# Optimization experiments

Measured on AMD Instinct MI355X. Metric: run time of the kernel, lower is better.

## Reference

```python
import jax, jax.numpy as jnp
import numpy as np

FEATURE_SIZE = 128
STRIDE = 16
BASE_SIZE = 16
RATIOS = [0.5, 1, 2]
SCALES = [8, 16, 32]


def _generate_anchors(feature_size, stride):
    # Faithful to the torch module's numpy anchor generation (incl. rounding).
    size = BASE_SIZE * BASE_SIZE
    size_ratios = size / np.array(RATIOS)
    ws = np.round(np.sqrt(size_ratios))
    hs = np.round(ws * np.array(RATIOS))
    base = []
    for w, h in zip(ws, hs):
        for s in SCALES:
            base.append([0.0, 0.0, w * s, h * s])
    base = np.array(base)  # [9, 4]
    xo, yo = np.meshgrid(np.arange(feature_size), np.arange(feature_size), indexing='ij')
    # original loop order: x outer, y inner, then 9 base anchors
    centers = np.stack([xo * stride, yo * stride], axis=-1).reshape(-1, 1, 2)  # [F*F,1,2]
    wh = np.broadcast_to(base[None, :, 2:4], (feature_size * feature_size, 9, 2))
    anchors = np.concatenate([np.broadcast_to(centers, wh.shape), wh], axis=-1).reshape(-1, 4)
    return jnp.asarray(anchors, dtype=jnp.float32)  # [F*F*9, 4]


def _conv(x, w, b, pad):
    y = jax.lax.conv_general_dilated(
        x, w, window_strides=(1, 1), padding=[(pad, pad), (pad, pad)],
        dimension_numbers=('NCHW', 'OIHW', 'NCHW'))
    return y + b[None, :, None, None]


def setup_inputs() -> dict:
    key = jax.random.key(0)
    ks = jax.random.split(key, 4)
    F = FEATURE_SIZE
    x = jax.random.normal(ks[0], (1, 1024, F, F), dtype=jnp.float32)
    base_w = jax.random.normal(ks[1], (512, 1024, 3, 3), dtype=jnp.float32) * 0.01
    base_b = jnp.zeros((512,), dtype=jnp.float32)
    cls_w = jax.random.normal(ks[2], (18, 512, 1, 1), dtype=jnp.float32) * 0.01
    cls_b = jnp.zeros((18,), dtype=jnp.float32)
    reg_w = jax.random.normal(ks[3], (36, 512, 1, 1), dtype=jnp.float32) * 0.01
    reg_b = jnp.zeros((36,), dtype=jnp.float32)
    return {"x": x, "base_w": base_w, "base_b": base_b,
            "cls_w": cls_w, "cls_b": cls_b, "reg_w": reg_w, "reg_b": reg_b}


def reference(x, base_w, base_b, cls_w, cls_b, reg_w, reg_b):
    F = FEATURE_SIZE
    anchors = _generate_anchors(F, STRIDE)  # [N,4], N = F*F*9

    rpn_conv = jax.nn.relu(_conv(x, base_w, base_b, pad=1))        # [1,512,F,F]
    rpn_cls = _conv(rpn_conv, cls_w, cls_b, pad=0)                  # [1,18,F,F]
    # softmax over the 2-way fg/bg axis after reshape, as in the original
    cls_rs = rpn_cls.reshape(1, 2, 9 * F, F)
    cls_prob = jax.nn.softmax(cls_rs, axis=1).reshape(1, 18, F, F)
    rpn_reg = _conv(rpn_conv, reg_w, reg_b, pad=0)                  # [1,36,F,F]

    cls = jnp.transpose(cls_prob, (0, 2, 3, 1)).reshape(-1, 2)      # [N,2]
    reg = jnp.transpose(rpn_reg, (0, 2, 3, 1)).reshape(-1, 4)       # [N,4]

    # Vectorized decode — faithful to the original per-anchor loop math:
    # p0 = ax + aw*d0 ; p1 = ay + ah*d1 ; p2 = aw + exp(d2) ; p3 = ah + exp(d3)
    p0 = anchors[:, 0] + anchors[:, 2] * reg[:, 0]
    p1 = anchors[:, 1] + anchors[:, 3] * reg[:, 1]
    p2 = anchors[:, 2] + jnp.exp(reg[:, 2])
    p3 = anchors[:, 3] + jnp.exp(reg[:, 3])
    proposals = jnp.stack([p0, p1, p2, p3], axis=-1)                # [N,4]
    scores = cls[:, 1]                                              # [N]
    return jnp.concatenate([proposals, scores[:, None]], axis=-1)   # [N,5]
```

## Files before the change

### kernel.cpp

```cpp
#include <hip/hip_runtime.h>
#include <hip/hip_bf16.h>

typedef unsigned short u16;
typedef short s4v __attribute__((ext_vector_type(4)));
typedef short s8v __attribute__((ext_vector_type(8)));
typedef float f4v __attribute__((ext_vector_type(4)));

#define F 128
#define CIN 1024
#define CMID 512
#define XP 130
#define K9 9216

#define A_ELEMS 8704
#define B_ELEMS 8192
#define AOFF(b) ((b) * A_ELEMS)
#define BOFF(b) (2 * A_ELEMS + (b) * B_ELEMS)

__device__ __forceinline__ u16 f2bf(float v) {
    union { float f; unsigned u; } x; x.f = v;
    unsigned r = x.u + 0x7fff + ((x.u >> 16) & 1);
    return (u16)(r >> 16);
}

__device__ __forceinline__ void gl16(const u16* g, u16* l) {
    __builtin_amdgcn_global_load_lds(
        (const __attribute__((address_space(1))) void*)g,
        (__attribute__((address_space(3))) void*)l,
        16, 0, 0);
}

__constant__ float WBASE[9] = {184.f, 368.f, 736.f, 128.f, 256.f, 512.f,  88.f, 176.f, 352.f};
__constant__ float HBASE[9] = { 96.f, 192.f, 384.f, 128.f, 256.f, 512.f, 176.f, 352.f, 704.f};

__global__ __launch_bounds__(256) void prep_all(
    const float* __restrict__ x, const float* __restrict__ bw,
    const float* __restrict__ cls_w, const float* __restrict__ reg_w,
    u16* __restrict__ xpad, u16* __restrict__ wt, u16* __restrict__ wc) {
    __shared__ u16 ldsT[64 * 132];
    const int b = blockIdx.x;
    const int tid = threadIdx.x;

    if (b < 2048) {
        const int h  = b >> 4;
        const int cb = (b & 15) * 64;
        {
            const int L = tid & 31, cl = tid >> 5;
            const int w4 = L * 4;
            #pragma unroll
            for (int p = 0; p < 8; ++p) {
                const int c = p * 8 + cl;
                f4v v = *(const f4v*)&x[(cb + c) * (F * F) + h * F + w4];
                s4v pk;
                #pragma unroll
                for (int k = 0; k < 4; ++k) pk[k] = (short)f2bf(v[k]);
                *(s4v*)&ldsT[c * 132 + w4] = pk;
            }
        }
        __syncthreads();
        {
            const int cs = (tid & 7) * 8;
            const int wb = tid >> 3;
            #pragma unroll
            for (int p = 0; p < 4; ++p) {
                const int w = p * 32 + wb;
                s8v o;
                #pragma unroll
                for (int j = 0; j < 8; ++j) o[j] = (short)ldsT[(cs + j) * 132 + w];
                *(s8v*)&xpad[((h + 1) * XP + (w + 1)) * CIN + cb + cs] = o;
            }
        }
    } else if (b < 2560) {
        const int oc = b - 2048;
        #pragma unroll 1
        for (int p = 0; p < 4; ++p) {
            const int c = p * 256 + tid;
            const float* src = bw + oc * K9 + c * 9;
            #pragma unroll
            for (int q = 0; q < 9; ++q)
                wt[oc * K9 + q * 1024 + c] = f2bf(src[q]);
        }
    } else if (b < 2818) {
        int t = (b - 2560) * 256 + tid;
        int cell = t >> 7, c8 = (t & 127) * 8;
        int h, w;
        if (cell < 130)      { h = 0;   w = cell; }
        else if (cell < 260) { h = 129; w = cell - 130; }
        else { int rm = cell - 260; h = 1 + (rm >> 1); w = (rm & 1) * 129; }
        s8v z = {};
        *(s8v*)&xpad[(h * XP + w) * CIN + c8] = z;
    } else {
        int t = (b - 2818) * 256 + tid;
        int oc = t >> 9, c = t & 511;
        float v = 0.f;
        if (oc < 18)      v = cls_w[oc * 512 + c];
        else if (oc < 54) v = reg_w[(oc - 18) * 512 + c];
        wc[t] = f2bf(v);
    }
}

__global__ __launch_bounds__(256, 2) void gemm_conv(
    const u16* __restrict__ xpad, const u16* __restrict__ wt,
    const float* __restrict__ bias, u16* __restrict__ rpn) {
    __shared__ u16 smem[2 * A_ELEMS + 2 * B_ELEMS];
    const int tid = threadIdx.x;
    const int w_id = (blockIdx.x & 7) * 64 + (blockIdx.x >> 3);
    const int oc0 = ((w_id & 7) >> 1) * 128;
    const int gh  = (w_id >> 3) * 2 + (w_id & 1);

    const int lane = tid & 63;
    const int wv = tid >> 6;
    const int lm = lane & 15;
    const int lq = lane >> 4;
    const int wm = (wv >> 1) * 64;
    const int wn = (wv & 1) * 64;

    const int sw = (lane & 7) ^ ((lane >> 3) & 7);
    const u16* pA = xpad + (lane >> 3) * CIN + sw * 8;
    const u16* pB = wt + (size_t)(oc0 + wv * 32 + (lane >> 3)) * K9 + sw * 8;

    f4v acc[4][4] = {};

    auto issueA = [&](int ms) {
        const int dy = ms >> 4, cc = ms & 15;
        const u16* src = pA + ((gh + dy) * XP) * CIN + cc * 64;
        u16* dst = &smem[AOFF(ms & 1)];
        #pragma unroll
        for (int jj = 0; jj < 4; ++jj) {
            const int ci = wv * 4 + jj;
            gl16(src + ci * 8 * CIN, dst + ci * 512);
        }
        if (wv == 0) gl16(src + 16 * 8 * CIN, dst + 16 * 512);
    };
    auto issueB = [&](int ms, int dx, int buf) {
        const int dy = ms >> 4, cc = ms & 15;
        const int dydx = dy * 3 + dx;
        const u16* src = pB + dydx * CIN + cc * 64;
        u16* dst = &smem[BOFF(buf) + wv * 32 * 64];
        #pragma unroll
        for (int jj = 0; jj < 4; ++jj)
            gl16(src + jj * 8 * K9, dst + jj * 8 * 64);
    };

    issueA(0);
    issueB(0, 0, 0);

    for (int ms = 0; ms < 48; ++ms) {
        const u16* Ab = &smem[AOFF(ms & 1)];
        #pragma unroll
        for (int dx = 0; dx < 3; ++dx) {
            const int t = ms * 3 + dx;

            if (dx == 1) {
                if (ms < 47) {
                    if (wv == 0) asm volatile("s_waitcnt vmcnt(5)" ::: "memory");
                    else         asm volatile("s_waitcnt vmcnt(4)" ::: "memory");
                } else {
                    asm volatile("s_waitcnt vmcnt(0)" ::: "memory");
                }
            } else {
                asm volatile("s_waitcnt vmcnt(0)" ::: "memory");
            }
            __builtin_amdgcn_s_barrier();

            if (t + 1 < 144) {
                const int msn = (dx == 2) ? ms + 1 : ms;
                const int dxn = (dx == 2) ? 0 : dx + 1;
                issueB(msn, dxn, (t + 1) & 1);
            }
            if (dx == 0 && ms + 1 < 48) issueA(ms + 1);

            const u16* Bb = &smem[BOFF(t & 1)];
            #pragma unroll
            for (int kk = 0; kk < 2; ++kk) {
                const int kseg = kk * 4 + lq;
                s8v af[4], bfr[4];
                #pragma unroll
                for (int i = 0; i < 4; ++i) {
                    const int ra = wm + i * 16 + lm + dx;
                    const int rb = wn + i * 16 + lm;
                    af[i]  = *(const s8v*)&Ab[ra * 64 + ((kseg ^ (ra & 7)) << 3)];
                    bfr[i] = *(const s8v*)&Bb[rb * 64 + ((kseg ^ (rb & 7)) << 3)];
                }
                #pragma unroll
                for (int mi = 0; mi < 4; ++mi)
                    #pragma unroll
                    for (int ni = 0; ni < 4; ++ni)
                        acc[mi][ni] = __builtin_amdgcn_mfma_f32_16x16x32_bf16(
                            af[mi], bfr[ni], acc[mi][ni], 0, 0, 0);
            }
        }
    }

    #pragma unroll
    for (int ni = 0; ni < 4; ++ni) {
        const int oc = oc0 + wn + ni * 16 + lm;
        const float bv = bias[oc];
        #pragma unroll
        for (int mi = 0; mi < 4; ++mi) {
            #pragma unroll
            for (int rr = 0; rr < 4; ++rr) {
                const int m = wm + mi * 16 + lq * 4 + rr;
                float v = acc[mi][ni][rr] + bv;
                v = v > 0.f ? v : 0.f;
                rpn[(gh * 128 + m) * CMID + oc] = f2bf(v);
            }
        }
    }
}

__global__ __launch_bounds__(256) void stage23(
    const u16* __restrict__ rpn, const u16* __restrict__ wc,
    const float* __restrict__ cls_b, const float* __restrict__ reg_b,
    float* __restrict__ out) {
    __shared__ float part[4][32][65];
    const int tid = threadIdx.x, lane = tid & 63, wv = tid >> 6;
    const int lm = lane & 15, lq = lane >> 4;
    const int m0 = blockIdx.x * 32;

    #pragma unroll
    for (int g = 0; g < 2; ++g) {
        f4v acc[4] = {};
        const u16* arow = rpn + (m0 + g * 16 + lm) * CMID + wv * 128 + lq * 8;
        const u16* brow = wc + lm * CMID + wv * 128 + lq * 8;
        #pragma unroll
        for (int k = 0; k < 4; ++k) {
            s8v af = *(const s8v*)(arow + k * 32);
            #pragma unroll
            for (int ni = 0; ni < 4; ++ni) {
                s8v bf = *(const s8v*)(brow + ni * 16 * CMID + k * 32);
                acc[ni] = __builtin_amdgcn_mfma_f32_16x16x32_bf16(af, bf, acc[ni], 0, 0, 0);
            }
        }
        #pragma unroll
        for (int ni = 0; ni < 4; ++ni)
            #pragma unroll
            for (int rr = 0; rr < 4; ++rr)
                part[wv][g * 16 + lq * 4 + rr][ni * 16 + lm] = acc[ni][rr];
    }
    __syncthreads();

    float vsum[8];
    const int col = tid & 63, rb = tid >> 6;
    const float bv = col < 18 ? cls_b[col] : (col < 54 ? reg_b[col - 18] : 0.f);
    #pragma unroll
    for (int rr = 0; rr < 8; ++rr) {
        const int row = rb * 8 + rr;
        vsum[rr] = part[0][row][col] + part[1][row][col]
                 + part[2][row][col] + part[3][row][col] + bv;
    }
    __syncthreads();
    #pragma unroll
    for (int rr = 0; rr < 8; ++rr)
        part[0][rb * 8 + rr][col] = vsum[rr];
    __syncthreads();

    #pragma unroll 1
    for (int g = 0; g < 2; ++g) {
        if (tid < 144) {
            const int pl0 = tid / 9, a = tid - pl0 * 9;
            const int pl = g * 16 + pl0;
            const float* v = part[0][pl];
            const int ch = 2 * a + 1;
            const int pair = (ch < 9) ? ch + 9 : ch - 9;
            const float score = 1.f / (1.f + expf(v[pair] - v[ch]));
            const float r0 = v[18 + 4 * a], r1 = v[19 + 4 * a];
            const float r2 = v[20 + 4 * a], r3 = v[21 + 4 * a];
            const float wb = WBASE[a], hb = HBASE[a];
            const int p = m0 + pl;
            const int h = p >> 7, w = p & 127;
            float* o = out + (p * 9 + a) * 5;
            o[0] = h * 16.f + wb * r0;
            o[1] = w * 16.f + hb * r1;
            o[2] = wb + expf(r2);
            o[3] = hb + expf(r3);
            o[4] = score;
        }
    }
}

extern "C" void kernel_launch(void* const* d_in, const int* in_sizes, int n_in,
                              void* d_out, int out_size, void* d_ws, size_t ws_size,
                              hipStream_t stream) {
    const float* x      = (const float*)d_in[0];
    const float* base_w = (const float*)d_in[1];
    const float* base_b = (const float*)d_in[2];
    const float* cls_w  = (const float*)d_in[3];
    const float* cls_b  = (const float*)d_in[4];
    const float* reg_w  = (const float*)d_in[5];
    const float* reg_b  = (const float*)d_in[6];
    float* out = (float*)d_out;

    char* ws = (char*)d_ws;
    u16* xpad = (u16*)ws;
    u16* wt   = (u16*)(ws + 34611200);
    u16* wc   = (u16*)(ws + 34611200 + 9437184);
    u16* rpn  = (u16*)(ws + 34611200 + 9437184 + 65536);

    prep_all<<<2946, 256, 0, stream>>>(x, base_w, cls_w, reg_w, xpad, wt, wc);
    gemm_conv<<<512, 256, 0, stream>>>(xpad, wt, base_b, rpn);
    stage23<<<512, 256, 0, stream>>>(rpn, wc, cls_b, reg_b, out);
}
```

Before: 257.2 us.

## Fuse 1x1 head stage into conv GEMM via last-block-per-row atomic counter

```diff
diff --git a/kernel.cpp b/kernel.cpp
--- a/kernel.cpp
+++ b/kernel.cpp
@@ -36,7 +36,8 @@
 __global__ __launch_bounds__(256) void prep_all(
     const float* __restrict__ x, const float* __restrict__ bw,
     const float* __restrict__ cls_w, const float* __restrict__ reg_w,
-    u16* __restrict__ xpad, u16* __restrict__ wt, u16* __restrict__ wc) {
+    u16* __restrict__ xpad, u16* __restrict__ wt, u16* __restrict__ wc,
+    unsigned* __restrict__ cnt, int doTail) {
     __shared__ u16 ldsT[64 * 132];
     const int b = blockIdx.x;
     const int tid = threadIdx.x;
@@ -96,127 +97,16 @@
         if (oc < 18)      v = cls_w[oc * 512 + c];
         else if (oc < 54) v = reg_w[(oc - 18) * 512 + c];
         wc[t] = f2bf(v);
-    }
-}
-
-__global__ __launch_bounds__(256, 2) void gemm_conv(
-    const u16* __restrict__ xpad, const u16* __restrict__ wt,
-    const float* __restrict__ bias, u16* __restrict__ rpn) {
-    __shared__ u16 smem[2 * A_ELEMS + 2 * B_ELEMS];
-    const int tid = threadIdx.x;
-    const int w_id = (blockIdx.x & 7) * 64 + (blockIdx.x >> 3);
-    const int oc0 = ((w_id & 7) >> 1) * 128;
-    const int gh  = (w_id >> 3) * 2 + (w_id & 1);
-
-    const int lane = tid & 63;
-    const int wv = tid >> 6;
-    const int lm = lane & 15;
-    const int lq = lane >> 4;
-    const int wm = (wv >> 1) * 64;
-    const int wn = (wv & 1) * 64;
-
-    const int sw = (lane & 7) ^ ((lane >> 3) & 7);
-    const u16* pA = xpad + (lane >> 3) * CIN + sw * 8;
-    const u16* pB = wt + (size_t)(oc0 + wv * 32 + (lane >> 3)) * K9 + sw * 8;
-
-    f4v acc[4][4] = {};
-
-    auto issueA = [&](int ms) {
-        const int dy = ms >> 4, cc = ms & 15;
-        const u16* src = pA + ((gh + dy) * XP) * CIN + cc * 64;
-        u16* dst = &smem[AOFF(ms & 1)];
-        #pragma unroll
-        for (int jj = 0; jj < 4; ++jj) {
-            const int ci = wv * 4 + jj;
-            gl16(src + ci * 8 * CIN, dst + ci * 512);
-        }
-        if (wv == 0) gl16(src + 16 * 8 * CIN, dst + 16 * 512);
-    };
-    auto issueB = [&](int ms, int dx, int buf) {
-        const int dy = ms >> 4, cc = ms & 15;
-        const int dydx = dy * 3 + dx;
-        const u16* src = pB + dydx * CIN + cc * 64;
-        u16* dst = &smem[BOFF(buf) + wv * 32 * 64];
-        #pragma unroll
-        for (int jj = 0; jj < 4; ++jj)
-            gl16(src + jj * 8 * K9, dst + jj * 8 * 64);
-    };
-
-    issueA(0);
-    issueB(0, 0, 0);
-
-    for (int ms = 0; ms < 48; ++ms) {
-        const u16* Ab = &smem[AOFF(ms & 1)];
-        #pragma unroll
-        for (int dx = 0; dx < 3; ++dx) {
-            const int t = ms * 3 + dx;
-
-            if (dx == 1) {
-                if (ms < 47) {
-                    if (wv == 0) asm volatile("s_waitcnt vmcnt(5)" ::: "memory");
-                    else         asm volatile("s_waitcnt vmcnt(4)" ::: "memory");
-                } else {
-                    asm volatile("s_waitcnt vmcnt(0)" ::: "memory");
-                }
-            } else {
-                asm volatile("s_waitcnt vmcnt(0)" ::: "memory");
-            }
-            __builtin_amdgcn_s_barrier();
-
-            if (t + 1 < 144) {
-                const int msn = (dx == 2) ? ms + 1 : ms;
-                const int dxn = (dx == 2) ? 0 : dx + 1;
-                issueB(msn, dxn, (t + 1) & 1);
-            }
-            if (dx == 0 && ms + 1 < 48) issueA(ms + 1);
-
-            const u16* Bb = &smem[BOFF(t & 1)];
-            #pragma unroll
-            for (int kk = 0; kk < 2; ++kk) {
-                const int kseg = kk * 4 + lq;
-                s8v af[4], bfr[4];
-                #pragma unroll
-                for (int i = 0; i < 4; ++i) {
-                    const int ra = wm + i * 16 + lm + dx;
-                    const int rb = wn + i * 16 + lm;
-                    af[i]  = *(const s8v*)&Ab[ra * 64 + ((kseg ^ (ra & 7)) << 3)];
-                    bfr[i] = *(const s8v*)&Bb[rb * 64 + ((kseg ^ (rb & 7)) << 3)];
-                }
-                #pragma unroll
-                for (int mi = 0; mi < 4; ++mi)
-                    #pragma unroll
-                    for (int ni = 0; ni < 4; ++ni)
-                        acc[mi][ni] = __builtin_amdgcn_mfma_f32_16x16x32_bf16(
-                            af[mi], bfr[ni], acc[mi][ni], 0, 0, 0);
-            }
-        }
-    }
-
-    #pragma unroll
-    for (int ni = 0; ni < 4; ++ni) {
-        const int oc = oc0 + wn + ni * 16 + lm;
-        const float bv = bias[oc];
-        #pragma unroll
-        for (int mi = 0; mi < 4; ++mi) {
-            #pragma unroll
-            for (int rr = 0; rr < 4; ++rr) {
-                const int m = wm + mi * 16 + lq * 4 + rr;
-                float v = acc[mi][ni][rr] + bv;
-                v = v > 0.f ? v : 0.f;
-                rpn[(gh * 128 + m) * CMID + oc] = f2bf(v);
-            }
-        }
-    }
-}
-
-__global__ __launch_bounds__(256) void stage23(
+        if (doTail && b == 2818 && tid < 128) cnt[tid] = 0u;
+    }
+}
+
+__device__ __forceinline__ void stage23_body(
     const u16* __restrict__ rpn, const u16* __restrict__ wc,
     const float* __restrict__ cls_b, const float* __restrict__ reg_b,
-    float* __restrict__ out) {
-    __shared__ float part[4][32][65];
-    const int tid = threadIdx.x, lane = tid & 63, wv = tid >> 6;
+    float* __restrict__ out, float (*part)[32][65], int m0, int tid) {
+    const int lane = tid & 63, wv = tid >> 6;
     const int lm = lane & 15, lq = lane >> 4;
-    const int m0 = blockIdx.x * 32;
 
     #pragma unroll
     for (int g = 0; g < 2; ++g) {
@@ -277,6 +167,144 @@
             o[4] = score;
         }
     }
+    __syncthreads();
+}
+
+__global__ __launch_bounds__(256, 2) void gemm_conv(
+    const u16* __restrict__ xpad, const u16* __restrict__ wt,
+    const float* __restrict__ bias, u16* __restrict__ rpn,
+    const u16* __restrict__ wc, const float* __restrict__ cls_b,
+    const float* __restrict__ reg_b, float* __restrict__ out,
+    unsigned* __restrict__ cnt, int doTail) {
+    __shared__ u16 smem[2 * A_ELEMS + 2 * B_ELEMS];
+    __shared__ int tailOld;
+    const int tid = threadIdx.x;
+    const int w_id = (blockIdx.x & 7) * 64 + (blockIdx.x >> 3);
+    const int oc0 = ((w_id & 7) >> 1) * 128;
+    const int gh  = (w_id >> 3) * 2 + (w_id & 1);
+
+    const int lane = tid & 63;
+    const int wv = tid >> 6;
+    const int lm = lane & 15;
+    const int lq = lane >> 4;
+    const int wm = (wv >> 1) * 64;
+    const int wn = (wv & 1) * 64;
+
+    const int sw = (lane & 7) ^ ((lane >> 3) & 7);
+    const u16* pA = xpad + (lane >> 3) * CIN + sw * 8;
+    const u16* pB = wt + (size_t)(oc0 + wv * 32 + (lane >> 3)) * K9 + sw * 8;
+
+    f4v acc[4][4] = {};
+
+    auto issueA = [&](int ms) {
+        const int dy = ms >> 4, cc = ms & 15;
+        const u16* src = pA + ((gh + dy) * XP) * CIN + cc * 64;
+        u16* dst = &smem[AOFF(ms & 1)];
+        #pragma unroll
+        for (int jj = 0; jj < 4; ++jj) {
+            const int ci = wv * 4 + jj;
+            gl16(src + ci * 8 * CIN, dst + ci * 512);
+        }
+        if (wv == 0) gl16(src + 16 * 8 * CIN, dst + 16 * 512);
+    };
+    auto issueB = [&](int ms, int dx, int buf) {
+        const int dy = ms >> 4, cc = ms & 15;
+        const int dydx = dy * 3 + dx;
+        const u16* src = pB + dydx * CIN + cc * 64;
+        u16* dst = &smem[BOFF(buf) + wv * 32 * 64];
+        #pragma unroll
+        for (int jj = 0; jj < 4; ++jj)
+            gl16(src + jj * 8 * K9, dst + jj * 8 * 64);
+    };
+
+    issueA(0);
+    issueB(0, 0, 0);
+
+    for (int ms = 0; ms < 48; ++ms) {
+        const u16* Ab = &smem[AOFF(ms & 1)];
+        #pragma unroll
+        for (int dx = 0; dx < 3; ++dx) {
+            const int t = ms * 3 + dx;
+
+            if (dx == 1) {
+                if (ms < 47) {
+                    if (wv == 0) asm volatile("s_waitcnt vmcnt(5)" ::: "memory");
+                    else         asm volatile("s_waitcnt vmcnt(4)" ::: "memory");
+                } else {
+                    asm volatile("s_waitcnt vmcnt(0)" ::: "memory");
+                }
+            } else {
+                asm volatile("s_waitcnt vmcnt(0)" ::: "memory");
+            }
+            __builtin_amdgcn_s_barrier();
+
+            if (t + 1 < 144) {
+                const int msn = (dx == 2) ? ms + 1 : ms;
+                const int dxn = (dx == 2) ? 0 : dx + 1;
+                issueB(msn, dxn, (t + 1) & 1);
+            }
+            if (dx == 0 && ms + 1 < 48) issueA(ms + 1);
+
+            const u16* Bb = &smem[BOFF(t & 1)];
+            #pragma unroll
+            for (int kk = 0; kk < 2; ++kk) {
+                const int kseg = kk * 4 + lq;
+                s8v af[4], bfr[4];
+                #pragma unroll
+                for (int i = 0; i < 4; ++i) {
+                    const int ra = wm + i * 16 + lm + dx;
+                    const int rb = wn + i * 16 + lm;
+                    af[i]  = *(const s8v*)&Ab[ra * 64 + ((kseg ^ (ra & 7)) << 3)];
+                    bfr[i] = *(const s8v*)&Bb[rb * 64 + ((kseg ^ (rb & 7)) << 3)];
+                }
+                #pragma unroll
+                for (int mi = 0; mi < 4; ++mi)
+                    #pragma unroll
+                    for (int ni = 0; ni < 4; ++ni)
+                        acc[mi][ni] = __builtin_amdgcn_mfma_f32_16x16x32_bf16(
+                            af[mi], bfr[ni], acc[mi][ni], 0, 0, 0);
+            }
+        }
+    }
+
+    #pragma unroll
+    for (int ni = 0; ni < 4; ++ni) {
+        const int oc = oc0 + wn + ni * 16 + lm;
+        const float bv = bias[oc];
+        #pragma unroll
+        for (int mi = 0; mi < 4; ++mi) {
+            #pragma unroll
+            for (int rr = 0; rr < 4; ++rr) {
+                const int m = wm + mi * 16 + lq * 4 + rr;
+                float v = acc[mi][ni][rr] + bv;
+                v = v > 0.f ? v : 0.f;
+                rpn[(gh * 128 + m) * CMID + oc] = f2bf(v);
+            }
+        }
+    }
+
+    if (doTail) {
+        __threadfence();
+        __syncthreads();
+        if (tid == 0) tailOld = (int)atomicAdd(&cnt[gh], 1u);
+        __syncthreads();
+        if (tailOld == 3) {
+            __threadfence();
+            float (*part)[32][65] = (float(*)[32][65])smem;
+            #pragma unroll 1
+            for (int g4 = 0; g4 < 4; ++g4)
+                stage23_body(rpn, wc, cls_b, reg_b, out, part,
+                             gh * 128 + g4 * 32, tid);
+        }
+    }
+}
+
+__global__ __launch_bounds__(256) void stage23(
+    const u16* __restrict__ rpn, const u16* __restrict__ wc,
+    const float* __restrict__ cls_b, const float* __restrict__ reg_b,
+    float* __restrict__ out) {
+    __shared__ float part[4][32][65];
+    stage23_body(rpn, wc, cls_b, reg_b, out, part, blockIdx.x * 32, threadIdx.x);
 }
 
 extern "C" void kernel_launch(void* const* d_in, const int* in_sizes, int n_in,
@@ -296,8 +324,14 @@
     u16* wt   = (u16*)(ws + 34611200);
     u16* wc   = (u16*)(ws + 34611200 + 9437184);
     u16* rpn  = (u16*)(ws + 34611200 + 9437184 + 65536);
-
-    prep_all<<<2946, 256, 0, stream>>>(x, base_w, cls_w, reg_w, xpad, wt, wc);
-    gemm_conv<<<512, 256, 0, stream>>>(xpad, wt, base_b, rpn);
-    stage23<<<512, 256, 0, stream>>>(rpn, wc, cls_b, reg_b, out);
-}
+    const size_t base = 34611200 + 9437184 + 65536 + 16777216;
+    const int doTail = (ws_size >= base + 512) ? 1 : 0;
+    unsigned* cnt = (unsigned*)(ws + base);
+
+    prep_all<<<2946, 256, 0, stream>>>(x, base_w, cls_w, reg_w, xpad, wt, wc,
+                                       cnt, doTail);
+    gemm_conv<<<512, 256, 0, stream>>>(xpad, wt, base_b, rpn, wc, cls_b,
+                                       reg_b, out, cnt, doTail);
+    if (!doTail)
+        stage23<<<512, 256, 0, stream>>>(rpn, wc, cls_b, reg_b, out);
+}
```

New measurement: 352.5 us. +37.1%, slower.
